# Kernel optimization log

Hardware: AMD Instinct MI355X
Metric: run time of the kernel (lower is better)

The kernel has to match this reference:

```python
import jax, jax.numpy as jnp
import numpy as np

B, H, L, D = 2, 16, 2048, 128


def setup_inputs() -> dict:
    key = jax.random.key(0)
    kq, kk, kv = jax.random.split(key, 3)
    q = jax.random.normal(kq, (B, H, L, D), dtype=jnp.float32)
    k = jax.random.normal(kk, (B, H, L, D), dtype=jnp.float32)
    v = jax.random.normal(kv, (B, H, L, D), dtype=jnp.float32)
    return {"q": q, "k": k, "v": v}


def reference(q, k, v):
    # Causal prefill attention (flash_attn_varlen_func / SDPA is_causal=True path).
    # q, k, v: [B, H, L, D]; scale = 1/sqrt(D) as in the fallback and constructor.
    Lq = q.shape[2]
    Dh = q.shape[3]
    scale = 1.0 / jnp.sqrt(jnp.asarray(Dh, q.dtype))
    scores = jnp.einsum('bhqd,bhkd->bhqk', q, k) * scale  # [B,H,Lq,Lk]
    causal = jnp.tril(jnp.ones((Lq, Lq), dtype=bool))      # [Lq,Lk]
    scores = jnp.where(causal, scores, jnp.finfo(q.dtype).min)
    probs = jax.nn.softmax(scores, axis=-1)
    return jnp.einsum('bhqk,bhkd->bhqd', probs, v)          # [B,H,Lq,D]
```

## Files before the change

### kernel.cpp

```cpp
#include <hip/hip_runtime.h>
#include <hip/hip_bf16.h>
#include <stdint.h>


#define BB 2
#define HH 16
#define LL 2048
#define DD 128

typedef float f32x4 __attribute__((ext_vector_type(4)));
typedef __bf16 bf16x8 __attribute__((ext_vector_type(8)));
typedef __bf16 bf16x2t __attribute__((ext_vector_type(2)));

union Frag16 {
    uint4    u;
    bf16x8   b;
    uint16_t s[8];
    uint32_t w32[4];
};

__device__ inline uint32_t pk2bf(float x, float y) {
    bf16x2t v;
    v.x = (__bf16)x;
    v.y = (__bf16)y;
    return __builtin_bit_cast(uint32_t, v);
}

__device__ inline uint16_t f2bf(float x) {
    uint32_t u = __builtin_bit_cast(uint32_t, x);
    u += 0x7fffu + ((u >> 16) & 1u);
    return (uint16_t)(u >> 16);
}

__device__ inline float fast_exp2(float x) {
#if __has_builtin(__builtin_amdgcn_exp2f)
    return __builtin_amdgcn_exp2f(x);
#else
    return exp2f(x);
#endif
}

__global__ __launch_bounds__(256) void conv_kv(
    const float* __restrict__ Kg, const float* __restrict__ Vg,
    uint4* __restrict__ Kf, uint4* __restrict__ Vf)
{
    const int bid = blockIdx.x;
    const int t   = threadIdx.x;
    if (bid < 2048) {
        const int unit = bid;
        #pragma unroll
        for (int i = 0; i < 2; ++i) {
            const int local = t + i * 256;
            const int tile  = unit * 2 + (local >> 8);
            const int c     = local & 255;
            const int ds = c >> 6, quad = (c >> 4) & 3, n16 = c & 15;
            const float* p = Kg + ((size_t)tile * 16 + n16) * DD + ds * 32 + quad * 8;
            float4 a = *(const float4*)p;
            float4 b = *(const float4*)(p + 4);
            Frag16 f;
            f.w32[0] = pk2bf(a.x, a.y); f.w32[1] = pk2bf(a.z, a.w);
            f.w32[2] = pk2bf(b.x, b.y); f.w32[3] = pk2bf(b.z, b.w);
            Kf[(size_t)tile * 256 + c] = f.u;
        }
    } else {
        const int g = bid - 2048;
        const int n16 = t & 15, dt = (t >> 4) & 7, quadH = t >> 7;
        #pragma unroll
        for (int qi = 0; qi < 2; ++qi) {
            const int quad = quadH + 2 * qi;
            const float* base = Vg + ((size_t)g * 32 + quad * 8) * DD + dt * 16 + n16;
            float v[8];
            #pragma unroll
            for (int j = 0; j < 8; ++j) v[j] = base[(size_t)j * DD];
            Frag16 f;
            f.w32[0] = pk2bf(v[0], v[1]); f.w32[1] = pk2bf(v[2], v[3]);
            f.w32[2] = pk2bf(v[4], v[5]); f.w32[3] = pk2bf(v[6], v[7]);
            Vf[(size_t)g * 512 + dt * 64 + quad * 16 + n16] = f.u;
        }
    }
}

__global__ __launch_bounds__(256, 2) void fa_main(
    const float* __restrict__ Qg, const uint4* __restrict__ Kf,
    const uint4* __restrict__ Vf, float* __restrict__ Og)
{
    __shared__ __align__(16) uint16_t Plds[4][16 * 40];
    __shared__ float Obuf[2][16 * 132];
    __shared__ float Lbuf[2][16];

    const int tid   = threadIdx.x;
    const int lane  = tid & 63;
    const int w     = tid >> 6;
    const int n16   = lane & 15;
    const int quad  = lane >> 4;
    const int qhalf = w & 1;
    const int kvway = w >> 1;

    const int i     = blockIdx.x;
    const int xcd   = i & 7;
    const int j     = i >> 3;
    const int pair  = j & 31;
    const int bh    = xcd * 4 + (j >> 5);

    constexpr float kC   = 0.08838834764831845f * 1.4426950408889634f;
    constexpr float kOff = -16.0f * 1.4426950408889634f;

    const uint4* kpb = Kf + (size_t)(bh * 128) * 256 + lane;
    const uint4* vpb = Vf + (size_t)(bh * 64) * 512 + lane;
    float* Oh = Og + (size_t)bh * LL * DD;

    #pragma unroll
    for (int phase = 0; phase < 2; ++phase) {
        const int P32    = phase ? 63 - pair : pair;
        const int q0     = P32 * 32;
        const int q_base = q0 + qhalf * 16;

        Frag16 qf[4];
        {
            const float* qrow = Qg + ((size_t)bh * LL + q_base + n16) * DD;
            #pragma unroll
            for (int ds = 0; ds < 4; ++ds) {
                const int d0 = ds * 32 + quad * 8;
                float4 a = *(const float4*)(qrow + d0);
                float4 b = *(const float4*)(qrow + d0 + 4);
                qf[ds].w32[0] = pk2bf(a.x, a.y); qf[ds].w32[1] = pk2bf(a.z, a.w);
                qf[ds].w32[2] = pk2bf(b.x, b.y); qf[ds].w32[3] = pk2bf(b.z, b.w);
            }
        }

        f32x4 oacc[8];
        #pragma unroll
        for (int dt = 0; dt < 8; ++dt) oacc[dt] = (f32x4)0.0f;
        float lpart = 0.0f;

        const int nt = P32 + 1;

        for (int t = kvway; t < nt; t += 2) {
            const int kv0 = t << 5;
            const uint4* kp = kpb + (size_t)(t * 2) * 256;
            const uint4* vp = vpb + (size_t)t * 512;

            f32x4 sacc[2] = {(f32x4)0.0f, (f32x4)0.0f};
            Frag16 kf[2][4];
            #pragma unroll
            for (int kt = 0; kt < 2; ++kt)
                #pragma unroll
                for (int ds = 0; ds < 4; ++ds) kf[kt][ds].u = kp[kt * 256 + ds * 64];
            __builtin_amdgcn_s_setprio(1);
            #pragma unroll
            for (int ds = 0; ds < 4; ++ds) {
                sacc[0] = __builtin_amdgcn_mfma_f32_16x16x32_bf16(kf[0][ds].b, qf[ds].b, sacc[0], 0, 0, 0);
                sacc[1] = __builtin_amdgcn_mfma_f32_16x16x32_bf16(kf[1][ds].b, qf[ds].b, sacc[1], 0, 0, 0);
            }
            __builtin_amdgcn_s_setprio(0);

            Frag16 vf[8];
            #pragma unroll
            for (int dt = 0; dt < 8; ++dt) vf[dt].u = vp[dt * 64];

            if (kv0 + 31 > q_base) {
                const int qg_ = q_base + n16;
                #pragma unroll
                for (int kt = 0; kt < 2; ++kt) {
                    const int kvg = kv0 + kt * 16 + quad * 4;
                    #pragma unroll
                    for (int r = 0; r < 4; ++r)
                        if (kvg + r > qg_) sacc[kt][r] = -1e30f;
                }
            }

            #pragma unroll
            for (int kt = 0; kt < 2; ++kt) {
                float p0 = fast_exp2(fmaf(sacc[kt][0], kC, kOff));
                float p1 = fast_exp2(fmaf(sacc[kt][1], kC, kOff));
                float p2 = fast_exp2(fmaf(sacc[kt][2], kC, kOff));
                float p3 = fast_exp2(fmaf(sacc[kt][3], kC, kOff));
                lpart += (p0 + p1) + (p2 + p3);
                uint2 pw;
                pw.x = pk2bf(p0, p1);
                pw.y = pk2bf(p2, p3);
                *(uint2*)&Plds[w][n16 * 40 + kt * 16 + quad * 4] = pw;
            }

            Frag16 pf;
            pf.u = *(const uint4*)&Plds[w][n16 * 40 + quad * 8];
            __builtin_amdgcn_s_setprio(1);
            #pragma unroll
            for (int dt = 0; dt < 8; ++dt)
                oacc[dt] = __builtin_amdgcn_mfma_f32_16x16x32_bf16(
                    pf.b, vf[dt].b, oacc[dt], 0, 0, 0);
            __builtin_amdgcn_s_setprio(0);
        }

        float lsum = lpart;
        lsum += __shfl_xor(lsum, 16);
        lsum += __shfl_xor(lsum, 32);

        if (kvway == 1) {
            if (lane < 16) Lbuf[qhalf][lane] = lsum;
            #pragma unroll
            for (int dt = 0; dt < 8; ++dt)
                #pragma unroll
                for (int r = 0; r < 4; ++r)
                    Obuf[qhalf][(quad * 4 + r) * 132 + dt * 16 + n16] = oacc[dt][r];
        }
        __syncthreads();
        if (kvway == 0) {
            lsum += Lbuf[qhalf][n16];
            #pragma unroll
            for (int r = 0; r < 4; ++r) {
                const float inv = 1.0f / __shfl(lsum, quad * 4 + r);
                const float* obr = &Obuf[qhalf][(quad * 4 + r) * 132 + n16];
                float* orow = Oh + (size_t)(q_base + quad * 4 + r) * DD + n16;
                #pragma unroll
                for (int dt = 0; dt < 8; ++dt)
                    orow[dt * 16] = (oacc[dt][r] + obr[dt * 16]) * inv;
            }
        }
        __syncthreads();
    }
}

__global__ __launch_bounds__(256) void fa_fallback(
    const float* __restrict__ Qg, const float* __restrict__ Kg,
    const float* __restrict__ Vg, float* __restrict__ Og)
{
    __shared__ uint4 Klds[32 * 16];
    __shared__ uint4 Vlds[128 * 4];
    __shared__ __align__(16) uint16_t Plds[4][32 * 40];

    const int tid  = threadIdx.x;
    const int lane = tid & 63;
    const int w    = tid >> 6;
    const int n16  = lane & 15;
    const int quad = lane >> 4;

    const int bh     = blockIdx.y;
    const int q0     = (gridDim.x - 1 - blockIdx.x) * 128;
    const int q_base = q0 + w * 32;

    const size_t base = (size_t)bh * LL * DD;
    const float* Qh = Qg + base;
    const float* Kh = Kg + base;
    const float* Vh = Vg + base;
    float*       Oh = Og + base;

    constexpr float kC = 0.08838834764831845f * 1.4426950408889634f;

    Frag16 qf[2][4];
    #pragma unroll
    for (int qt = 0; qt < 2; ++qt) {
        const float* qrow = Qh + (size_t)(q_base + qt * 16 + n16) * DD;
        #pragma unroll
        for (int ds = 0; ds < 4; ++ds) {
            const int d0 = ds * 32 + quad * 8;
            float4 a = *(const float4*)(qrow + d0);
            float4 b = *(const float4*)(qrow + d0 + 4);
            Frag16 f;
            f.s[0] = f2bf(a.x); f.s[1] = f2bf(a.y); f.s[2] = f2bf(a.z); f.s[3] = f2bf(a.w);
            f.s[4] = f2bf(b.x); f.s[5] = f2bf(b.y); f.s[6] = f2bf(b.z); f.s[7] = f2bf(b.w);
            qf[qt][ds] = f;
        }
    }

    f32x4 oacc[2][8];
    #pragma unroll
    for (int qt = 0; qt < 2; ++qt)
        #pragma unroll
        for (int dt = 0; dt < 8; ++dt) oacc[qt][dt] = (f32x4)0.0f;
    float mrow[2] = {-1e30f, -1e30f};
    float lrow[2] = {0.0f, 0.0f};

    const int ntiles = q0 / 32 + 4;

    for (int t = 0; t < ntiles; ++t) {
        const int kv0 = t * 32;
        __syncthreads();
        #pragma unroll
        for (int iu = 0; iu < 2; ++iu) {
            const int cid = tid + iu * 256;
            const int r = cid >> 4, c = cid & 15;
            const float* src = Kh + (size_t)(kv0 + r) * DD + c * 8;
            float4 a = *(const float4*)src;
            float4 b = *(const float4*)(src + 4);
            Frag16 f;
            f.s[0] = f2bf(a.x); f.s[1] = f2bf(a.y); f.s[2] = f2bf(a.z); f.s[3] = f2bf(a.w);
            f.s[4] = f2bf(b.x); f.s[5] = f2bf(b.y); f.s[6] = f2bf(b.z); f.s[7] = f2bf(b.w);
            Klds[r * 16 + (c ^ (r & 7))] = f.u;
        }
        #pragma unroll
        for (int iu = 0; iu < 2; ++iu) {
            const int cid = tid + iu * 256;
            const int d = cid >> 2, ch = cid & 3;
            const float* src = Vh + (size_t)(kv0 + ch * 8) * DD + d;
            Frag16 f;
            #pragma unroll
            for (int j = 0; j < 8; ++j) f.s[j] = f2bf(src[(size_t)j * DD]);
            Vlds[d * 4 + (ch ^ ((d >> 1) & 3))] = f.u;
        }
        __syncthreads();

        if (kv0 > q_base + 31) continue;

        f32x4 sacc[2][2];
        #pragma unroll
        for (int kt = 0; kt < 2; ++kt)
            #pragma unroll
            for (int qt = 0; qt < 2; ++qt) sacc[kt][qt] = (f32x4)0.0f;

        #pragma unroll
        for (int ds = 0; ds < 4; ++ds) {
            Frag16 kfr[2];
            #pragma unroll
            for (int kt = 0; kt < 2; ++kt) {
                const int r = kt * 16 + n16;
                const int c = ds * 4 + quad;
                kfr[kt].u = Klds[r * 16 + (c ^ (r & 7))];
            }
            #pragma unroll
            for (int kt = 0; kt < 2; ++kt)
                #pragma unroll
                for (int qt = 0; qt < 2; ++qt)
                    sacc[kt][qt] = __builtin_amdgcn_mfma_f32_16x16x32_bf16(
                        kfr[kt].b, qf[qt][ds].b, sacc[kt][qt], 0, 0, 0);
        }

        if (kv0 + 31 > q_base) {
            #pragma unroll
            for (int kt = 0; kt < 2; ++kt) {
                const int kvg = kv0 + kt * 16 + quad * 4;
                #pragma unroll
                for (int qt = 0; qt < 2; ++qt) {
                    const int qg_ = q_base + qt * 16 + n16;
                    #pragma unroll
                    for (int r = 0; r < 4; ++r)
                        if (kvg + r > qg_) sacc[kt][qt][r] = -1e30f;
                }
            }
        }

        #pragma unroll
        for (int qt = 0; qt < 2; ++qt) {
            float mt = sacc[0][qt][0];
            #pragma unroll
            for (int kt = 0; kt < 2; ++kt)
                #pragma unroll
                for (int r = 0; r < 4; ++r) mt = fmaxf(mt, sacc[kt][qt][r]);
            mt = fmaxf(mt, __shfl_xor(mt, 16));
            mt = fmaxf(mt, __shfl_xor(mt, 32));
            const float mnew  = fmaxf(mrow[qt], mt);
            const float alpha = exp2f((mrow[qt] - mnew) * kC);
            mrow[qt] = mnew;

            float ls = 0.0f;
            uint16_t* prow = &Plds[w][(qt * 16 + n16) * 40];
            #pragma unroll
            for (int kt = 0; kt < 2; ++kt)
                #pragma unroll
                for (int r = 0; r < 4; ++r) {
                    const float p = exp2f((sacc[kt][qt][r] - mnew) * kC);
                    ls += p;
                    prow[kt * 16 + quad * 4 + r] = f2bf(p);
                }
            ls += __shfl_xor(ls, 16);
            ls += __shfl_xor(ls, 32);
            lrow[qt] = lrow[qt] * alpha + ls;

            #pragma unroll
            for (int r = 0; r < 4; ++r) {
                const float ar = __shfl(alpha, quad * 4 + r);
                #pragma unroll
                for (int dt = 0; dt < 8; ++dt) oacc[qt][dt][r] *= ar;
            }
        }

        Frag16 pfr[2];
        #pragma unroll
        for (int qt = 0; qt < 2; ++qt)
            pfr[qt].u = *(const uint4*)&Plds[w][(qt * 16 + n16) * 40 + quad * 8];
        #pragma unroll
        for (int dt = 0; dt < 8; ++dt) {
            const int d = dt * 16 + n16;
            Frag16 vfr;
            vfr.u = Vlds[d * 4 + (quad ^ ((d >> 1) & 3))];
            #pragma unroll
            for (int qt = 0; qt < 2; ++qt)
                oacc[qt][dt] = __builtin_amdgcn_mfma_f32_16x16x32_bf16(
                    pfr[qt].b, vfr.b, oacc[qt][dt], 0, 0, 0);
        }
    }

    #pragma unroll
    for (int qt = 0; qt < 2; ++qt) {
        #pragma unroll
        for (int r = 0; r < 4; ++r) {
            const float lr  = __shfl(lrow[qt], quad * 4 + r);
            const float inv = 1.0f / lr;
            const int row = q_base + qt * 16 + quad * 4 + r;
            float* orow = Oh + (size_t)row * DD + n16;
            #pragma unroll
            for (int dt = 0; dt < 8; ++dt)
                orow[dt * 16] = oacc[qt][dt][r] * inv;
        }
    }
}

extern "C" void kernel_launch(void* const* d_in, const int* in_sizes, int n_in,
                              void* d_out, int out_size, void* d_ws, size_t ws_size,
                              hipStream_t stream) {
    const float* q = (const float*)d_in[0];
    const float* k = (const float*)d_in[1];
    const float* v = (const float*)d_in[2];
    float* o = (float*)d_out;

    const size_t TENS = (size_t)BB * HH * LL * DD * 2;
    if (ws_size >= 2 * TENS) {
        uint4* Kf = (uint4*)d_ws;
        uint4* Vf = (uint4*)((char*)d_ws + TENS);
        conv_kv<<<dim3(4096), dim3(256), 0, stream>>>(k, v, Kf, Vf);
        fa_main<<<dim3(1024), dim3(256), 0, stream>>>(q, Kf, Vf, o);
    } else {
        fa_fallback<<<dim3(16, BB * HH), dim3(256), 0, stream>>>(q, k, v, o);
    }
}
```

Before: 197.7 us.

## Share double-buffered K/V LDS tiles across four query warps per block

Each block now handles a 64-row query tile with four warps on separate 16-row slices. The warps share K/V tiles staged into double-buffered LDS through global_load_lds, replacing per-warp direct global loads. The intent is to cut redundant global/L2 traffic for K and V and overlap the next tile's load with compute. The split-KV reduction through LDS is removed, and the grid is halved to 512 blocks. The cost is a block-wide barrier every KV iteration, fewer blocks, and warps in the lower query slices doing fully masked work on the diagonal tiles.

```diff
diff --git a/kernel.cpp b/kernel.cpp
--- a/kernel.cpp
+++ b/kernel.cpp
@@ -38,6 +38,12 @@
 #else
     return exp2f(x);
 #endif
+}
+
+__device__ __forceinline__ void stage16(const uint4* g, uint4* l) {
+    __builtin_amdgcn_global_load_lds(
+        (const __attribute__((address_space(1))) unsigned int*)g,
+        (__attribute__((address_space(3))) unsigned int*)l, 16, 0, 0);
 }
 
 __global__ __launch_bounds__(256) void conv_kv(
@@ -84,36 +90,35 @@
     const float* __restrict__ Qg, const uint4* __restrict__ Kf,
     const uint4* __restrict__ Vf, float* __restrict__ Og)
 {
+    __shared__ __align__(16) uint4 Klds[2][512];
+    __shared__ __align__(16) uint4 Vlds[2][512];
     __shared__ __align__(16) uint16_t Plds[4][16 * 40];
-    __shared__ float Obuf[2][16 * 132];
-    __shared__ float Lbuf[2][16];
-
-    const int tid   = threadIdx.x;
-    const int lane  = tid & 63;
-    const int w     = tid >> 6;
-    const int n16   = lane & 15;
-    const int quad  = lane >> 4;
-    const int qhalf = w & 1;
-    const int kvway = w >> 1;
-
-    const int i     = blockIdx.x;
-    const int xcd   = i & 7;
-    const int j     = i >> 3;
-    const int pair  = j & 31;
-    const int bh    = xcd * 4 + (j >> 5);
+
+    const int tid  = threadIdx.x;
+    const int lane = tid & 63;
+    const int w    = tid >> 6;
+    const int n16  = lane & 15;
+    const int quad = lane >> 4;
+
+    const int i    = blockIdx.x;
+    const int xcd  = i & 7;
+    const int j    = i >> 3;
+    const int pair = j & 15;
+    const int bh   = xcd * 4 + (j >> 4);
 
     constexpr float kC   = 0.08838834764831845f * 1.4426950408889634f;
     constexpr float kOff = -16.0f * 1.4426950408889634f;
 
-    const uint4* kpb = Kf + (size_t)(bh * 128) * 256 + lane;
-    const uint4* vpb = Vf + (size_t)(bh * 64) * 512 + lane;
     float* Oh = Og + (size_t)bh * LL * DD;
+
+    const int kq_off = (w >> 1) * 256 + ((w & 1) * 2) * 64;
+    const int vq_off = (2 * w) * 64;
 
     #pragma unroll
     for (int phase = 0; phase < 2; ++phase) {
-        const int P32    = phase ? 63 - pair : pair;
-        const int q0     = P32 * 32;
-        const int q_base = q0 + qhalf * 16;
+        const int qtile  = phase ? pair : 31 - pair;
+        const int q0     = qtile * 64;
+        const int q_base = q0 + w * 16;
 
         Frag16 qf[4];
         {
@@ -133,19 +138,41 @@
         for (int dt = 0; dt < 8; ++dt) oacc[dt] = (f32x4)0.0f;
         float lpart = 0.0f;
 
-        const int nt = P32 + 1;
-
-        for (int t = kvway; t < nt; t += 2) {
+        const int nt = 2 * qtile + 2;
+
+        {
+            const uint4* kg = Kf + ((size_t)(bh * 128) * 256) + kq_off + lane;
+            const uint4* vg = Vf + ((size_t)(bh * 64) * 512) + vq_off + lane;
+            stage16(kg,      &Klds[0][kq_off]);
+            stage16(kg + 64, &Klds[0][kq_off + 64]);
+            stage16(vg,      &Vlds[0][vq_off]);
+            stage16(vg + 64, &Vlds[0][vq_off + 64]);
+        }
+        __syncthreads();
+
+        int cur = 0;
+        for (int t = 0; t < nt; ++t) {
+            if (t + 1 < nt) {
+                const uint4* kg = Kf + ((size_t)(bh * 128 + 2 * (t + 1)) * 256) + kq_off + lane;
+                const uint4* vg = Vf + ((size_t)(bh * 64 + (t + 1)) * 512) + vq_off + lane;
+                uint4* kd = &Klds[cur ^ 1][kq_off];
+                uint4* vd = &Vlds[cur ^ 1][vq_off];
+                stage16(kg,      kd);
+                stage16(kg + 64, kd + 64);
+                stage16(vg,      vd);
+                stage16(vg + 64, vd + 64);
+            }
+
+            const uint4* Kl = Klds[cur];
+            const uint4* Vl = Vlds[cur];
             const int kv0 = t << 5;
-            const uint4* kp = kpb + (size_t)(t * 2) * 256;
-            const uint4* vp = vpb + (size_t)t * 512;
 
             f32x4 sacc[2] = {(f32x4)0.0f, (f32x4)0.0f};
             Frag16 kf[2][4];
             #pragma unroll
             for (int kt = 0; kt < 2; ++kt)
                 #pragma unroll
-                for (int ds = 0; ds < 4; ++ds) kf[kt][ds].u = kp[kt * 256 + ds * 64];
+                for (int ds = 0; ds < 4; ++ds) kf[kt][ds].u = Kl[kt * 256 + ds * 64 + lane];
             __builtin_amdgcn_s_setprio(1);
             #pragma unroll
             for (int ds = 0; ds < 4; ++ds) {
@@ -156,7 +183,7 @@
 
             Frag16 vf[8];
             #pragma unroll
-            for (int dt = 0; dt < 8; ++dt) vf[dt].u = vp[dt * 64];
+            for (int dt = 0; dt < 8; ++dt) vf[dt].u = Vl[dt * 64 + lane];
 
             if (kv0 + 31 > q_base) {
                 const int qg_ = q_base + n16;
@@ -190,34 +217,22 @@
                 oacc[dt] = __builtin_amdgcn_mfma_f32_16x16x32_bf16(
                     pf.b, vf[dt].b, oacc[dt], 0, 0, 0);
             __builtin_amdgcn_s_setprio(0);
+
+            __syncthreads();
+            cur ^= 1;
         }
 
         float lsum = lpart;
         lsum += __shfl_xor(lsum, 16);
         lsum += __shfl_xor(lsum, 32);
-
-        if (kvway == 1) {
-            if (lane < 16) Lbuf[qhalf][lane] = lsum;
+        #pragma unroll
+        for (int r = 0; r < 4; ++r) {
+            const float inv = 1.0f / __shfl(lsum, quad * 4 + r);
+            float* orow = Oh + (size_t)(q_base + quad * 4 + r) * DD + n16;
             #pragma unroll
             for (int dt = 0; dt < 8; ++dt)
-                #pragma unroll
-                for (int r = 0; r < 4; ++r)
-                    Obuf[qhalf][(quad * 4 + r) * 132 + dt * 16 + n16] = oacc[dt][r];
-        }
-        __syncthreads();
-        if (kvway == 0) {
-            lsum += Lbuf[qhalf][n16];
-            #pragma unroll
-            for (int r = 0; r < 4; ++r) {
-                const float inv = 1.0f / __shfl(lsum, quad * 4 + r);
-                const float* obr = &Obuf[qhalf][(quad * 4 + r) * 132 + n16];
-                float* orow = Oh + (size_t)(q_base + quad * 4 + r) * DD + n16;
-                #pragma unroll
-                for (int dt = 0; dt < 8; ++dt)
-                    orow[dt * 16] = (oacc[dt][r] + obr[dt * 16]) * inv;
-            }
-        }
-        __syncthreads();
+                orow[dt * 16] = oacc[dt][r] * inv;
+        }
     }
 }
 
@@ -418,7 +433,7 @@
         uint4* Kf = (uint4*)d_ws;
         uint4* Vf = (uint4*)((char*)d_ws + TENS);
         conv_kv<<<dim3(4096), dim3(256), 0, stream>>>(k, v, Kf, Vf);
-        fa_main<<<dim3(1024), dim3(256), 0, stream>>>(q, Kf, Vf, o);
+        fa_main<<<dim3(512), dim3(256), 0, stream>>>(q, Kf, Vf, o);
     } else {
         fa_fallback<<<dim3(16, BB * HH), dim3(256), 0, stream>>>(q, k, v, o);
     }
```

Result: faster. 185.0 us (-6.5%).
